# Performance work log

Hardware: AMD Instinct MI355X
Metric: run time of the kernel (lower is better)

The kernel has to match this reference:

```python
import jax, jax.numpy as jnp
import numpy as np

# Mamba2(d_model=256, headdim=32) defaults: d_state=128, d_conv=4, expand=2, ngroups=1, chunk=256
B, CIN, L = 8, 256, 1024
D_MODEL = CIN
D_INNER = 2 * D_MODEL            # expand=2 -> 512
HEADDIM = 32
NHEADS = D_INNER // HEADDIM      # 16
D_STATE = 128
D_CONV = 4
CONV_DIM = D_INNER + 2 * D_STATE             # 768 (ngroups=1)
D_IN_PROJ = 2 * D_INNER + 2 * D_STATE + NHEADS  # 1296
GN_GROUPS = 8
CHUNK = 256
EPS = 1e-5

def setup_inputs():
    key = jax.random.key(0)
    ks = jax.random.split(key, 8)
    x = jax.random.normal(ks[0], (B, CIN, L), jnp.float32)
    W_in = jax.random.normal(ks[1], (D_IN_PROJ, D_MODEL), jnp.float32) * 0.02
    conv_w = jax.random.normal(ks[2], (CONV_DIM, D_CONV), jnp.float32) * 0.2
    conv_b = jax.random.normal(ks[3], (CONV_DIM,), jnp.float32) * 0.02
    dt = jnp.exp(jax.random.uniform(ks[4], (NHEADS,)) * (jnp.log(0.1) - jnp.log(0.001)) + jnp.log(0.001))
    dt_bias = dt + jnp.log(-jnp.expm1(-dt))   # inverse softplus
    A_log = jnp.log(jax.random.uniform(ks[5], (NHEADS,), minval=1.0, maxval=16.0))
    Dp = jnp.ones((NHEADS,), jnp.float32)
    rms_w = jnp.ones((D_INNER,), jnp.float32)
    W_out = jax.random.normal(ks[6], (D_MODEL, D_INNER), jnp.float32) * 0.02
    gn_w = jnp.ones((CIN,), jnp.float32)
    gn_b = jnp.zeros((CIN,), jnp.float32)
    return dict(x=x, W_in=W_in, conv_w=conv_w, conv_b=conv_b, dt_bias=dt_bias,
                A_log=A_log, Dp=Dp, rms_w=rms_w, W_out=W_out, gn_w=gn_w, gn_b=gn_b)

def segsum(a):
    # a: (..., T) -> (..., T, T) with sum_{j<i<=t} a_i on/below diagonal, -inf above
    T = a.shape[-1]
    cs = jnp.cumsum(a, -1)
    d = cs[..., :, None] - cs[..., None, :]
    mask = jnp.tril(jnp.ones((T, T), bool))
    return jnp.where(mask, d, -jnp.inf)

def ssd(X, A, Bm, Cm):
    # X: (b,l,h,p) already dt-scaled; A: (b,l,h) = dt*A_cont; Bm,Cm: (b,l,n) (ngroups=1)
    b, l, h, p = X.shape
    n = Bm.shape[-1]
    c = l // CHUNK
    X = X.reshape(b, c, CHUNK, h, p)
    A = A.reshape(b, c, CHUNK, h).transpose(0, 3, 1, 2)      # (b,h,c,l)
    Bm = Bm.reshape(b, c, CHUNK, n)
    Cm = Cm.reshape(b, c, CHUNK, n)
    A_cs = jnp.cumsum(A, -1)                                  # (b,h,c,l)
    Lmat = jnp.exp(segsum(A))                                 # (b,h,c,l,l)
    Y_diag = jnp.einsum('bcln,bcsn,bhcls,bcshp->bclhp', Cm, Bm, Lmat, X)
    decay_states = jnp.exp(A_cs[..., -1:] - A_cs)             # (b,h,c,l)
    states = jnp.einsum('bcln,bhcl,bclhp->bchpn', Bm, decay_states, X)
    decay_chunk = jnp.exp(segsum(jnp.pad(A_cs[..., -1], ((0, 0), (0, 0), (1, 0)))))  # (b,h,c+1,c+1)
    states = jnp.concatenate([jnp.zeros_like(states[:, :1]), states], axis=1)        # (b,c+1,h,p,n)
    prev = jnp.einsum('bhzc,bchpn->bzhpn', decay_chunk, states)[:, :-1]              # (b,c,h,p,n)
    Y_off = jnp.einsum('bcln,bchpn,bhcl->bclhp', Cm, prev, jnp.exp(A_cs))
    return (Y_diag + Y_off).reshape(b, l, h, p)

def _forward(x, W_in, conv_w, conv_b, dt_bias, A_log, Dp, rms_w, W_out, gn_w, gn_b):
    u = jnp.transpose(x, (0, 2, 1))                           # (B,L,d_model)
    zxbcdt = u @ W_in.T                                       # (B,L,1296)
    z = zxbcdt[..., :D_INNER]
    xBC = zxbcdt[..., D_INNER:D_INNER + CONV_DIM]
    dt = jax.nn.softplus(zxbcdt[..., D_INNER + CONV_DIM:] + dt_bias)  # (B,L,H)
    # causal depthwise conv1d + SiLU
    xpad = jnp.pad(xBC, ((0, 0), (D_CONV - 1, 0), (0, 0)))
    xconv = conv_b + sum(conv_w[:, k] * xpad[:, k:k + L, :] for k in range(D_CONV))
    xconv = jax.nn.silu(xconv)
    xs = xconv[..., :D_INNER].reshape(B, L, NHEADS, HEADDIM)
    Bm = xconv[..., D_INNER:D_INNER + D_STATE]
    Cm = xconv[..., D_INNER + D_STATE:]
    A = -jnp.exp(A_log)                                       # (H,)
    Y = ssd(dt[..., None] * xs, dt * A, Bm, Cm)               # (B,L,H,P)
    Y = Y + xs * Dp[None, None, :, None]
    # gated RMSNorm (norm_before_gate=False): rmsnorm(y * silu(z)) * weight
    y = Y.reshape(B, L, D_INNER) * jax.nn.silu(z)
    y = y * jax.lax.rsqrt(jnp.mean(y * y, -1, keepdims=True) + EPS) * rms_w
    out = jnp.transpose(y @ W_out.T, (0, 2, 1))               # (B,C,L)
    # GroupNorm(8, C) over (channels_per_group, L)
    og = out.reshape(B, GN_GROUPS, CIN // GN_GROUPS, L)
    mu = og.mean((2, 3), keepdims=True)
    var = og.var((2, 3), keepdims=True)
    out = ((og - mu) * jax.lax.rsqrt(var + EPS)).reshape(B, CIN, L)
    out = out * gn_w[None, :, None] + gn_b[None, :, None]
    return out * jnp.tanh(jax.nn.softplus(out))               # Mish

def reference(x, W_in, conv_w, conv_b, dt_bias, A_log, Dp, rms_w, W_out, gn_w, gn_b):
    return _forward(x, W_in, conv_w, conv_b, dt_bias, A_log, Dp, rms_w, W_out, gn_w, gn_b)
```

## Files before the change

### kernel.cpp

```cpp
#include <hip/hip_runtime.h>
#include <hip/hip_bf16.h>
#include <math.h>

#define B_ 8
#define L_ 1024
#define DM 256
#define DI 512
#define HD 32
#define NH 16
#define DS 128
#define CDIM 768
#define NZX 1280
#define CH 256
#define NC 4
#define M_ (B_*L_)
#define EPSV 1e-5f

typedef short bf16x8 __attribute__((ext_vector_type(8)));
typedef float f32x4 __attribute__((ext_vector_type(4)));

#define OFF_ZX   0
#define SZ_ZX    (M_*NZX/2)
#define OFF_XC   (OFF_ZX+SZ_ZX)
#define SZ_XC    (M_*CDIM/2)
#define OFF_DTP  (OFF_XC+SZ_XC)
#define SZ_DTP   (4*M_*NH)
#define OFF_ACS  (OFF_DTP+SZ_DTP)
#define SZ_ACS   (B_*NC*NH*CH)
#define OFF_S0   (OFF_ACS+SZ_ACS)
#define SZ_S0    (B_*NC*CH*CH/2)
#define OFF_ST   (OFF_S0+SZ_S0)
#define SZ_ST    (B_*NC*NH*HD*DS/2)
#define OFF_Y    (OFF_ST+SZ_ST)
#define SZ_Y     (M_*DI/2)
#define OFF_YNB  (OFF_Y+SZ_Y)
#define SZ_YNB   (M_*DI/2)
#define OFF_XBF  (OFF_YNB+SZ_YNB)
#define SZ_XBF   (M_*DM/2)
#define OFF_WBF  (OFF_XBF+SZ_XBF)
#define SZ_WBF   (1296*DM/2)
#define OFF_WOBF (OFF_WBF+SZ_WBF)
#define SZ_WOBF  (DM*DI/2)
#define OFF_GNP  (OFF_WOBF+SZ_WOBF)
#define SZ_GNP   (64*2)
#define OFF_BT   (OFF_GNP+SZ_GNP)
#define SZ_BT    (32*128*256/2)
#define OFF_OUTB (OFF_BT+SZ_BT)
#define SZ_OUTB  (M_*DM/2)

__device__ __forceinline__ ushort f2bf(float v) {
  __hip_bfloat16 h = __float2bfloat16(v);
  return *(ushort*)&h;
}
__device__ __forceinline__ float bf2f(ushort u) {
  return __uint_as_float(((unsigned int)u) << 16);
}
__device__ __forceinline__ float dt_load(const float* __restrict__ dtp, size_t di) {
  float s = dtp[di] + dtp[(size_t)M_*NH + di] + dtp[2*(size_t)M_*NH + di] + dtp[3*(size_t)M_*NH + di];
  return (s > 20.f) ? s : log1pf(expf(s));
}

__device__ __forceinline__ void gload16(const ushort* g, ushort* l) {
  __builtin_amdgcn_global_load_lds(
      (const __attribute__((address_space(1))) unsigned int*)g,
      (__attribute__((address_space(3))) unsigned int*)l,
      16, 0, 0);
}

__global__ __launch_bounds__(256) void k_prep(const float* __restrict__ x,
                                              const float* __restrict__ W_in,
                                              const float* __restrict__ W_out,
                                              const float* __restrict__ dt_bias,
                                              ushort* __restrict__ xbf,
                                              ushort* __restrict__ wbf,
                                              ushort* __restrict__ wobf,
                                              float2* __restrict__ gnp,
                                              float* __restrict__ dtp) {
  __shared__ float Ts[64][65];
  __shared__ float Wd[16][65];
  const int bid = blockIdx.x;
  const int t = threadIdx.x;
  if (bid < 512) {
    const int kt = bid & 3, lt2 = (bid >> 2) & 15, b = bid >> 6;
    const int k0 = kt*64, l0 = lt2*64;
    for (int i = t; i < 1024; i += 256) {
      int kk = i>>4, lw = i&15;
      float4 v = *(const float4*)&x[(size_t)b*DM*L_ + (size_t)(k0+kk)*L_ + l0 + lw*4];
      Ts[kk][lw*4+0] = v.x; Ts[kk][lw*4+1] = v.y;
      Ts[kk][lw*4+2] = v.z; Ts[kk][lw*4+3] = v.w;
    }
    for (int i = t; i < 1024; i += 256) {
      int h = i>>6, kk = i&63;
      Wd[h][kk] = W_in[(size_t)(NZX+h)*DM + k0+kk];
    }
    __syncthreads();
    for (int i = t; i < 512; i += 256) {
      int mm = i>>3, kg = i&7;
      union { ushort u[8]; uint4 q; } pk;
#pragma unroll
      for (int j = 0; j < 8; ++j) pk.u[j] = f2bf(Ts[kg*8+j][mm]);
      *(uint4*)&xbf[(size_t)(b*L_ + l0+mm)*DM + k0 + kg*8] = pk.q;
    }
    const int h = t&15, lg = t>>4;
    const float bias = (kt == 0) ? dt_bias[h] : 0.f;
#pragma unroll
    for (int c = 0; c < 4; ++c) {
      const int ll = lg + c*16;
      float acc = bias;
#pragma unroll 8
      for (int kk = 0; kk < 64; ++kk) acc += Wd[h][kk]*Ts[kk][ll];
      dtp[(size_t)kt*M_*NH + (size_t)(b*L_ + l0+ll)*NH + h] = acc;
    }
  } else if (bid < 512 + 1296) {
    int i = (bid-512)*256 + t;
    if (i < 1296*DM) wbf[i] = f2bf(W_in[i]);
  } else if (bid < 512 + 1296 + 512) {
    int i = (bid-512-1296)*256 + t;
    wobf[i] = f2bf(W_out[i]);
  } else {
    if (t < 64) gnp[t] = make_float2(0.f, 0.f);
  }
}

__global__ __launch_bounds__(256) void k_gemm_in_mfma(const ushort* __restrict__ xbf,
                                                      const ushort* __restrict__ wbf,
                                                      ushort* __restrict__ zxb) {
  __shared__ __attribute__((aligned(16))) ushort As[2][128*32];
  __shared__ __attribute__((aligned(16))) ushort Bs[2][128*32];
  const int tid = threadIdx.x;
  const int n0 = blockIdx.x*128, m0 = blockIdx.y*128;
  const int wave = tid>>6, lane = tid&63;
  const int lr = lane&15, quad = lane>>4;
  const int rA = lane>>2;
  const int cA = (lane&3)*8;
  f32x4 acc[2][8];
#pragma unroll
  for (int mi=0;mi<2;++mi)
#pragma unroll
    for (int ni=0;ni<8;++ni)
#pragma unroll
      for (int r=0;r<4;++r) acc[mi][ni][r] = 0.f;
  auto STAGE = [&](int buf, int k0) {
#pragma unroll
    for (int j = 0; j < 2; ++j) {
      const int ch = 2*wave + j;
      const int row = ch*16 + rA;
      gload16(xbf + (size_t)(m0+row)*DM + k0 + cA, &As[buf][ch*512]);
      gload16(wbf + (size_t)(n0+row)*DM + k0 + cA, &Bs[buf][ch*512]);
    }
  };
  STAGE(0, 0);
#pragma unroll
  for (int i = 0; i < 8; ++i) {
    __syncthreads();
    if (i < 7) STAGE((i+1)&1, (i+1)*32);
    const int cur = i&1;
    bf16x8 af[2], bfr[8];
    af[0] = *(const bf16x8*)&As[cur][(wave*32+lr)*32 + quad*8];
    af[1] = *(const bf16x8*)&As[cur][(wave*32+16+lr)*32 + quad*8];
#pragma unroll
    for (int ni=0;ni<8;++ni) bfr[ni] = *(const bf16x8*)&Bs[cur][(ni*16+lr)*32 + quad*8];
#pragma unroll
    for (int mi=0;mi<2;++mi)
#pragma unroll
      for (int ni=0;ni<8;++ni)
        acc[mi][ni] = __builtin_amdgcn_mfma_f32_16x16x32_bf16(af[mi], bfr[ni], acc[mi][ni], 0, 0, 0);
  }
#pragma unroll
  for (int mi=0;mi<2;++mi) {
    int m = m0 + wave*32 + mi*16 + quad*4;
#pragma unroll
    for (int ni=0;ni<8;++ni) {
      int n = n0 + ni*16 + lr;
#pragma unroll
      for (int r=0;r<4;++r) zxb[(size_t)(m+r)*NZX + n] = f2bf(acc[mi][ni][r]);
    }
  }
}

__global__ __launch_bounds__(256) void k_conv(const ushort* __restrict__ zxb,
                                              const float* __restrict__ cw,
                                              const float* __restrict__ cb,
                                              ushort* __restrict__ xcb,
                                              ushort* __restrict__ btg) {
  const int j = blockIdx.x*256 + threadIdx.x;
  const int m8 = blockIdx.y*8;
  const int l0 = m8 & 1023;
  const int mb = m8 & ~1023;
  const float4 w = *(const float4*)&cw[j*4];
  const float bias = cb[j];
  float v[11];
#pragma unroll
  for (int i = 0; i < 11; ++i) {
    int ll = l0 - 3 + i;
    v[i] = (ll >= 0) ? bf2f(zxb[(size_t)(mb+ll)*NZX + DI + j]) : 0.f;
  }
  union { ushort u[8]; uint4 q; } res;
#pragma unroll
  for (int i = 0; i < 8; ++i) {
    float a = bias + w.x*v[i] + w.y*v[i+1] + w.z*v[i+2] + w.w*v[i+3];
    a = a / (1.f + expf(-a));
    res.u[i] = f2bf(a);
    xcb[(size_t)(mb+l0+i)*CDIM + j] = res.u[i];
  }
  if (j >= DI && j < DI+DS) {
    const int n = j - DI;
    const int bc = (mb >> 10)*NC + (l0 >> 8);
    const int lc = l0 & 255;
    *(uint4*)&btg[((size_t)bc*DS + n)*CH + lc] = res.q;
  }
}

__global__ __launch_bounds__(256) void k_s0st(const ushort* __restrict__ xcb,
                                              const ushort* __restrict__ btg,
                                              const float* __restrict__ dtp,
                                              const float* __restrict__ A_log,
                                              float* __restrict__ acs_g,
                                              ushort* __restrict__ stb,
                                              ushort* __restrict__ S0b) {
  __shared__ float wtot[4];
  __shared__ ushort Xw[32][264];
  const int role = blockIdx.x;
  const int bc = blockIdx.y;
  const int base = bc*CH;
  const int t = threadIdx.x;
  const int wave = t>>6, lane = t&63, lr = lane&15, quad = lane>>4;
  if (role < 10) {
    const int lt = (role>=6) ? 3 : (role>=3) ? 2 : (role>=1) ? 1 : 0;
    const int st = role - lt*(lt+1)/2;
    const int l = lt*64 + wave*16 + lr;
    f32x4 acc[4];
#pragma unroll
    for (int nt = 0; nt < 4; ++nt)
#pragma unroll
      for (int r = 0; r < 4; ++r) acc[nt][r] = 0.f;
#pragma unroll
    for (int ks = 0; ks < 4; ++ks) {
      bf16x8 af = *(const bf16x8*)(xcb + (size_t)(base+l)*CDIM + (DI+DS) + ks*32 + quad*8);
#pragma unroll
      for (int nt = 0; nt < 4; ++nt) {
        bf16x8 bf = *(const bf16x8*)(xcb + (size_t)(base + st*64 + nt*16 + lr)*CDIM + DI + ks*32 + quad*8);
        acc[nt] = __builtin_amdgcn_mfma_f32_16x16x32_bf16(af, bf, acc[nt], 0, 0, 0);
      }
    }
    const bool diag = (lt == st);
#pragma unroll
    for (int nt = 0; nt < 4; ++nt)
#pragma unroll
      for (int r = 0; r < 4; ++r) {
        const int lrow = lt*64 + wave*16 + quad*4 + r;
        const int scol = st*64 + nt*16 + lr;
        ushort v = (!diag || scol <= lrow) ? f2bf(acc[nt][r]) : (ushort)0;
        S0b[((size_t)bc*CH + lrow)*CH + scol] = v;
      }
    return;
  }
  const int h = role - 10;
  float dt_t = dt_load(dtp, (size_t)(base+t)*NH + h);
  float An = -expf(A_log[h]);
  float v = dt_t * An;
#pragma unroll
  for (int off = 1; off < 64; off <<= 1) {
    float u = __shfl_up(v, off);
    if (lane >= off) v += u;
  }
  if (lane == 63) wtot[wave] = v;
  __syncthreads();
  float pre = 0.f, tot = 0.f;
#pragma unroll
  for (int wj = 0; wj < 4; ++wj) {
    float wv = wtot[wj];
    tot += wv;
    if (wj < wave) pre += wv;
  }
  const float a = v + pre;
  const float alast = tot;
  acs_g[((size_t)bc*NH + h)*CH + t] = a;
  float w = expf(alast - a) * dt_t;
  {
    const ushort* xp = xcb + (size_t)(base+t)*CDIM + h*HD;
    ushort tmp[32];
    *(uint4*)&tmp[0]  = *(const uint4*)(xp);
    *(uint4*)&tmp[8]  = *(const uint4*)(xp+8);
    *(uint4*)&tmp[16] = *(const uint4*)(xp+16);
    *(uint4*)&tmp[24] = *(const uint4*)(xp+24);
#pragma unroll
    for (int p = 0; p < 32; ++p) Xw[p][t] = f2bf(bf2f(tmp[p]) * w);
  }
  __syncthreads();
  f32x4 acc2[2][2];
#pragma unroll
  for (int mt=0;mt<2;++mt)
#pragma unroll
    for (int nt=0;nt<2;++nt)
#pragma unroll
      for (int r=0;r<4;++r) acc2[mt][nt][r] = 0.f;
  const ushort* bp = btg + (size_t)bc*DS*CH;
#pragma unroll
  for (int k0 = 0; k0 < CH; k0 += 32) {
    bf16x8 a0 = *(const bf16x8*)&Xw[lr][k0 + quad*8];
    bf16x8 a1 = *(const bf16x8*)&Xw[16+lr][k0 + quad*8];
    bf16x8 b0 = *(const bf16x8*)(bp + (size_t)(wave*32 + lr)*CH + k0 + quad*8);
    bf16x8 b1 = *(const bf16x8*)(bp + (size_t)(wave*32 + 16 + lr)*CH + k0 + quad*8);
    acc2[0][0] = __builtin_amdgcn_mfma_f32_16x16x32_bf16(a0, b0, acc2[0][0], 0,0,0);
    acc2[0][1] = __builtin_amdgcn_mfma_f32_16x16x32_bf16(a0, b1, acc2[0][1], 0,0,0);
    acc2[1][0] = __builtin_amdgcn_mfma_f32_16x16x32_bf16(a1, b0, acc2[1][0], 0,0,0);
    acc2[1][1] = __builtin_amdgcn_mfma_f32_16x16x32_bf16(a1, b1, acc2[1][1], 0,0,0);
  }
  size_t sb = ((size_t)bc*NH + h)*HD*DS;
#pragma unroll
  for (int mt = 0; mt < 2; ++mt)
#pragma unroll
    for (int nt = 0; nt < 2; ++nt)
#pragma unroll
      for (int r = 0; r < 4; ++r)
        stb[sb + (size_t)(mt*16 + quad*4 + r)*DS + wave*32 + nt*16 + lr] = f2bf(acc2[mt][nt][r]);
}

__global__ __launch_bounds__(256) void k_y_mfma(const ushort* __restrict__ xcb,
    const float* __restrict__ dtp, const float* __restrict__ acs_g,
    const ushort* __restrict__ S0b, const ushort* __restrict__ stb,
    const float* __restrict__ Dp, ushort* __restrict__ Yb) {
  __shared__ ushort Xt[32][280];
  __shared__ ushort Xs[32][280];
  __shared__ float acs[CH];
  const int t = threadIdx.x;
  const int bc = blockIdx.x, h = blockIdx.y;
  const int base = bc*CH;
  const int cc = bc & 3, bc4 = bc & ~3;
  acs[t] = acs_g[((size_t)bc*NH + h)*CH + t];
  const float dts_t = dt_load(dtp, (size_t)(base+t)*NH + h);
  ushort tmp[32];
  {
    const ushort* xp = xcb + (size_t)(base+t)*CDIM + h*HD;
    *(uint4*)&tmp[0]  = *(const uint4*)(xp);
    *(uint4*)&tmp[8]  = *(const uint4*)(xp+8);
    *(uint4*)&tmp[16] = *(const uint4*)(xp+16);
    *(uint4*)&tmp[24] = *(const uint4*)(xp+24);
#pragma unroll
    for (int p = 0; p < 32; ++p) Xt[p][t] = tmp[p];
  }
  __syncthreads();
  const float e32 = expf(acs[t & ~31] - acs[t]) * dts_t;
#pragma unroll
  for (int p = 0; p < 32; ++p) Xs[p][t] = f2bf(bf2f(tmp[p]) * e32);
  __syncthreads();
  const int wave = t>>6, lane = t&63, lr = lane&15, quad = lane>>4;
  f32x4 acc[4][2];
#pragma unroll
  for (int mt=0;mt<4;++mt)
#pragma unroll
    for (int nt=0;nt<2;++nt)
#pragma unroll
      for (int r=0;r<4;++r) acc[mt][nt][r] = 0.f;
  if (cc > 0) {
    float fj[3];
    {
      float cum = 0.f;
      for (int j = cc-1; j >= 0; --j) {
        fj[j] = expf(cum);
        cum += acs_g[((size_t)(bc4+j)*NH + h)*CH + (CH-1)];
      }
    }
#pragma unroll
    for (int ks = 0; ks < 4; ++ks) {
      bf16x8 bfr[2];
#pragma unroll
      for (int nt = 0; nt < 2; ++nt) {
        float P[8];
#pragma unroll
        for (int jj = 0; jj < 8; ++jj) P[jj] = 0.f;
        for (int j = 0; j < cc; ++j) {
          bf16x8 sv = *(const bf16x8*)(stb + ((size_t)(bc4+j)*NH + h)*HD*DS
                                       + (size_t)(nt*16+lr)*DS + ks*32 + quad*8);
#pragma unroll
          for (int jj = 0; jj < 8; ++jj) P[jj] += fj[j]*bf2f((ushort)sv[jj]);
        }
        bf16x8 bb;
#pragma unroll
        for (int jj = 0; jj < 8; ++jj) bb[jj] = (short)f2bf(P[jj]);
        bfr[nt] = bb;
      }
#pragma unroll
      for (int mt = 0; mt < 4; ++mt) {
        int l = mt*64 + wave*16 + lr;
        bf16x8 af = *(const bf16x8*)(xcb + (size_t)(base+l)*CDIM + (DI+DS) + ks*32 + quad*8);
        acc[mt][0] = __builtin_amdgcn_mfma_f32_16x16x32_bf16(af, bfr[0], acc[mt][0], 0,0,0);
        acc[mt][1] = __builtin_amdgcn_mfma_f32_16x16x32_bf16(af, bfr[1], acc[mt][1], 0,0,0);
      }
    }
    const float es0 = expf(acs[0]);
#pragma unroll
    for (int mt = 0; mt < 4; ++mt)
#pragma unroll
      for (int nt = 0; nt < 2; ++nt)
#pragma unroll
        for (int r = 0; r < 4; ++r) acc[mt][nt][r] *= es0;
  }
  const int Kw = (12 + wave) >> 1;
  for (int ks = 0; ks <= Kw; ++ks) {
    const int sq = ks*32;
    const bf16x8 xb0 = *(const bf16x8*)&Xs[lr][sq + quad*8];
    const bf16x8 xb1 = *(const bf16x8*)&Xs[16+lr][sq + quad*8];
    const float g = (ks > 0) ? expf(acs[sq] - acs[sq-32]) : 1.f;
#pragma unroll
    for (int mt = 0; mt < 4; ++mt) {
      const int rt = 4*mt + wave;
      if (ks > (rt>>1)) continue;
      if (ks > 0) {
#pragma unroll
        for (int r = 0; r < 4; ++r) { acc[mt][0][r] *= g; acc[mt][1][r] *= g; }
      }
      const int l = mt*64 + wave*16 + lr;
      const bf16x8 sb = *(const bf16x8*)(S0b + ((size_t)bc*CH + l)*CH + sq + quad*8);
      acc[mt][0] = __builtin_amdgcn_mfma_f32_16x16x32_bf16(sb, xb0, acc[mt][0], 0,0,0);
      acc[mt][1] = __builtin_amdgcn_mfma_f32_16x16x32_bf16(sb, xb1, acc[mt][1], 0,0,0);
    }
  }
  const float dph = Dp[h];
#pragma unroll
  for (int mt = 0; mt < 4; ++mt) {
    const int Kmt = (4*mt + wave) >> 1;
    const float aref = acs[32*Kmt];
    const int lb = mt*64 + wave*16 + quad*4;
#pragma unroll
    for (int r = 0; r < 4; ++r) {
      const float e = expf(acs[lb+r] - aref);
#pragma unroll
      for (int nt = 0; nt < 2; ++nt) {
        const int p = nt*16 + lr;
        float xv = bf2f(Xt[p][lb+r]);
        Yb[(size_t)(base+lb+r)*DI + h*HD + p] = f2bf(acc[mt][nt][r]*e + dph*xv);
      }
    }
  }
}

__global__ __launch_bounds__(256) void k_rms(const ushort* __restrict__ zxb,
                                             const ushort* __restrict__ Yb,
                                             const float* __restrict__ rw,
                                             ushort* __restrict__ yn) {
  const int m = blockIdx.x*4 + (threadIdx.x>>6);
  const int lane = threadIdx.x & 63;
  const int c0 = lane*8;
  bf16x8 zv = *(const bf16x8*)(zxb + (size_t)m*NZX + c0);
  bf16x8 yv = *(const bf16x8*)(Yb  + (size_t)m*DI  + c0);
  float y[8];
  float ss = 0.f;
#pragma unroll
  for (int j = 0; j < 8; ++j) {
    float z = bf2f((ushort)zv[j]);
    y[j] = bf2f((ushort)yv[j]) * z / (1.f + expf(-z));
    ss += y[j]*y[j];
  }
#pragma unroll
  for (int off = 1; off < 64; off <<= 1) ss += __shfl_xor(ss, off);
  const float inv = rsqrtf(ss * (1.f/DI) + EPSV);
  float4 w0 = *(const float4*)&rw[c0];
  float4 w1 = *(const float4*)&rw[c0+4];
  const float wv[8] = {w0.x,w0.y,w0.z,w0.w,w1.x,w1.y,w1.z,w1.w};
  union { ushort u[8]; uint4 q; } pk;
#pragma unroll
  for (int j = 0; j < 8; ++j) pk.u[j] = f2bf(y[j] * inv * wv[j]);
  *(uint4*)(yn + (size_t)m*DI + c0) = pk.q;
}

__global__ __launch_bounds__(256) void k_gemm_out_mfma(const ushort* __restrict__ ynbf,
                                                       const ushort* __restrict__ wobf,
                                                       ushort* __restrict__ outb,
                                                       float2* __restrict__ gnp) {
  __shared__ __attribute__((aligned(16))) ushort As[2][64*32];
  __shared__ __attribute__((aligned(16))) ushort Bs[2][128*32];
  __shared__ float red[4][8];
  const int tid = threadIdx.x;
  const int n0 = blockIdx.x*128, m0 = blockIdx.y*64;
  const int wave = tid>>6, lane = tid&63;
  const int lr = lane&15, quad = lane>>4;
  const int rA = lane>>2;
  const int cA = (lane&3)*8;
  f32x4 acc[8];
#pragma unroll
  for (int ni=0;ni<8;++ni)
#pragma unroll
    for (int r=0;r<4;++r) acc[ni][r] = 0.f;
  auto STAGE = [&](int buf, int k0) {
    gload16(ynbf + (size_t)(m0 + wave*16 + rA)*DI + k0 + cA, &As[buf][wave*512]);
#pragma unroll
    for (int j = 0; j < 2; ++j) {
      const int ch = 2*wave + j;
      gload16(wobf + (size_t)(n0 + ch*16 + rA)*DI + k0 + cA, &Bs[buf][ch*512]);
    }
  };
  STAGE(0, 0);
#pragma unroll
  for (int i = 0; i < 16; ++i) {
    __syncthreads();
    if (i < 15) STAGE((i+1)&1, (i+1)*32);
    const int cur = i&1;
    bf16x8 af = *(const bf16x8*)&As[cur][(wave*16+lr)*32 + quad*8];
    bf16x8 bfr[8];
#pragma unroll
    for (int ni=0;ni<8;++ni) bfr[ni] = *(const bf16x8*)&Bs[cur][(ni*16+lr)*32 + quad*8];
#pragma unroll
    for (int ni=0;ni<8;++ni)
      acc[ni] = __builtin_amdgcn_mfma_f32_16x16x32_bf16(af, bfr[ni], acc[ni], 0, 0, 0);
  }
  const int b = m0 >> 10, l0 = m0 & 1023;
  float sg[4] = {0.f,0.f,0.f,0.f}, sq2[4] = {0.f,0.f,0.f,0.f};
#pragma unroll
  for (int ni=0;ni<8;++ni) {
    int n = n0 + ni*16 + lr;
    union { ushort u[4]; uint2 q; } pk;
#pragma unroll
    for (int r=0;r<4;++r) pk.u[r] = f2bf(acc[ni][r]);
    *(uint2*)&outb[(size_t)b*DM*L_ + (size_t)n*L_ + l0 + wave*16 + quad*4] = pk.q;
    float ps = acc[ni][0]+acc[ni][1]+acc[ni][2]+acc[ni][3];
    float pq = acc[ni][0]*acc[ni][0]+acc[ni][1]*acc[ni][1]
             + acc[ni][2]*acc[ni][2]+acc[ni][3]*acc[ni][3];
    sg[ni>>1] += ps; sq2[ni>>1] += pq;
  }
#pragma unroll
  for (int g = 0; g < 4; ++g)
#pragma unroll
    for (int off = 32; off > 0; off >>= 1) {
      sg[g]  += __shfl_down(sg[g],  off);
      sq2[g] += __shfl_down(sq2[g], off);
    }
  if (lane == 0) {
#pragma unroll
    for (int g = 0; g < 4; ++g) { red[wave][g] = sg[g]; red[wave][4+g] = sq2[g]; }
  }
  __syncthreads();
  if (tid == 0) {
    int g0 = b*8 + (n0>>5);
#pragma unroll
    for (int g = 0; g < 4; ++g) {
      float S = red[0][g]+red[1][g]+red[2][g]+red[3][g];
      float Q = red[0][4+g]+red[1][4+g]+red[2][4+g]+red[3][4+g];
      atomicAdd(&gnp[g0+g].x, S);
      atomicAdd(&gnp[g0+g].y, Q);
    }
  }
}

__global__ __launch_bounds__(256) void k_gn_apply(const float2* __restrict__ gnp,
                                                  const float* __restrict__ gw,
                                                  const float* __restrict__ gb,
                                                  const ushort* __restrict__ ob,
                                                  float* __restrict__ o) {
  const int ch = blockIdx.x & 255, b = blockIdx.x >> 8;
  const int t = threadIdx.x;
  float2 p = gnp[b*8 + (ch>>5)];
  const float mean = p.x * (1.f/(32.f*L_));
  const float var  = p.y * (1.f/(32.f*L_)) - mean*mean;
  const float inv  = rsqrtf(var + EPSV);
  const float w = gw[ch], bb = gb[ch];
  size_t base = (size_t)blockIdx.x * L_;
  ushort4 v = *(const ushort4*)&ob[base + t*4];
  float r[4] = {bf2f(v.x), bf2f(v.y), bf2f(v.z), bf2f(v.w)};
#pragma unroll
  for (int j = 0; j < 4; ++j) {
    float u = (r[j] - mean) * inv * w + bb;
    float m;
    if (u > 15.f) m = u;
    else {
      float e = expf(u);
      float a = 1.f + e;
      float a2 = a*a;
      m = u * (a2 - 1.f) / (a2 + 1.f);
    }
    r[j] = m;
  }
  *(float4*)&o[base + t*4] = make_float4(r[0], r[1], r[2], r[3]);
}

extern "C" void kernel_launch(void* const* d_in, const int* in_sizes, int n_in,
                              void* d_out, int out_size, void* d_ws, size_t ws_size,
                              hipStream_t stream) {
  const float* x       = (const float*)d_in[0];
  const float* W_in    = (const float*)d_in[1];
  const float* conv_w  = (const float*)d_in[2];
  const float* conv_b  = (const float*)d_in[3];
  const float* dt_bias = (const float*)d_in[4];
  const float* A_log   = (const float*)d_in[5];
  const float* Dp      = (const float*)d_in[6];
  const float* rms_w   = (const float*)d_in[7];
  const float* W_out   = (const float*)d_in[8];
  const float* gn_w    = (const float*)d_in[9];
  const float* gn_b    = (const float*)d_in[10];
  float* out = (float*)d_out;
  float* ws  = (float*)d_ws;

  ushort* zxb   = (ushort*)(ws + OFF_ZX);
  ushort* xcb   = (ushort*)(ws + OFF_XC);
  float*  dtp   = ws + OFF_DTP;
  float*  acs   = ws + OFF_ACS;
  ushort* S0b   = (ushort*)(ws + OFF_S0);
  ushort* stb   = (ushort*)(ws + OFF_ST);
  ushort* Ybb   = (ushort*)(ws + OFF_Y);
  ushort* ynbf  = (ushort*)(ws + OFF_YNB);
  ushort* xbf   = (ushort*)(ws + OFF_XBF);
  ushort* wbf   = (ushort*)(ws + OFF_WBF);
  ushort* wobf  = (ushort*)(ws + OFF_WOBF);
  float2* gnp   = (float2*)(ws + OFF_GNP);
  ushort* btg   = (ushort*)(ws + OFF_BT);
  ushort* outb  = (ushort*)(ws + OFF_OUTB);

  k_prep         <<<dim3(512+1296+512+1), 256, 0, stream>>>(x, W_in, W_out, dt_bias,
                                                            xbf, wbf, wobf, gnp, dtp);
  k_gemm_in_mfma <<<dim3(NZX/128, M_/128), 256, 0, stream>>>(xbf, wbf, zxb);
  k_conv         <<<dim3(3, M_/8), 256, 0, stream>>>(zxb, conv_w, conv_b, xcb, btg);
  k_s0st         <<<dim3(26, B_*NC), 256, 0, stream>>>(xcb, btg, dtp, A_log, acs, stb, S0b);
  k_y_mfma       <<<dim3(B_*NC, NH), 256, 0, stream>>>(xcb, dtp, acs, S0b, stb, Dp, Ybb);
  k_rms          <<<dim3(M_/4), 256, 0, stream>>>(zxb, Ybb, rms_w, ynbf);
  k_gemm_out_mfma<<<dim3(DM/128, M_/64), 256, 0, stream>>>(ynbf, wobf, outb, gnp);
  k_gn_apply     <<<dim3(B_*DM), 256, 0, stream>>>(gnp, gn_w, gn_b, outb, out);
}
```

Baseline: 176.0 us.

## Fuse gated RMSNorm into output GEMM and transpose-store via shared memory

```diff
diff --git a/kernel.cpp b/kernel.cpp
--- a/kernel.cpp
+++ b/kernel.cpp
@@ -325,7 +325,7 @@
   __shared__ ushort Xs[32][280];
   __shared__ float acs[CH];
   const int t = threadIdx.x;
-  const int bc = blockIdx.x, h = blockIdx.y;
+  const int h = blockIdx.x, bc = blockIdx.y;
   const int base = bc*CH;
   const int cc = bc & 3, bc4 = bc & ~3;
   acs[t] = acs_g[((size_t)bc*NH + h)*CH + t];
@@ -436,91 +436,90 @@
   }
 }
 
-__global__ __launch_bounds__(256) void k_rms(const ushort* __restrict__ zxb,
-                                             const ushort* __restrict__ Yb,
-                                             const float* __restrict__ rw,
-                                             ushort* __restrict__ yn) {
-  const int m = blockIdx.x*4 + (threadIdx.x>>6);
-  const int lane = threadIdx.x & 63;
-  const int c0 = lane*8;
-  bf16x8 zv = *(const bf16x8*)(zxb + (size_t)m*NZX + c0);
-  bf16x8 yv = *(const bf16x8*)(Yb  + (size_t)m*DI  + c0);
-  float y[8];
-  float ss = 0.f;
-#pragma unroll
-  for (int j = 0; j < 8; ++j) {
-    float z = bf2f((ushort)zv[j]);
-    y[j] = bf2f((ushort)yv[j]) * z / (1.f + expf(-z));
-    ss += y[j]*y[j];
-  }
-#pragma unroll
-  for (int off = 1; off < 64; off <<= 1) ss += __shfl_xor(ss, off);
-  const float inv = rsqrtf(ss * (1.f/DI) + EPSV);
-  float4 w0 = *(const float4*)&rw[c0];
-  float4 w1 = *(const float4*)&rw[c0+4];
-  const float wv[8] = {w0.x,w0.y,w0.z,w0.w,w1.x,w1.y,w1.z,w1.w};
-  union { ushort u[8]; uint4 q; } pk;
-#pragma unroll
-  for (int j = 0; j < 8; ++j) pk.u[j] = f2bf(y[j] * inv * wv[j]);
-  *(uint4*)(yn + (size_t)m*DI + c0) = pk.q;
-}
-
-__global__ __launch_bounds__(256) void k_gemm_out_mfma(const ushort* __restrict__ ynbf,
-                                                       const ushort* __restrict__ wobf,
-                                                       ushort* __restrict__ outb,
-                                                       float2* __restrict__ gnp) {
-  __shared__ __attribute__((aligned(16))) ushort As[2][64*32];
+__global__ __launch_bounds__(256) void k_out_fused(const ushort* __restrict__ zxb,
+                                                   const ushort* __restrict__ Yb,
+                                                   const float* __restrict__ rw,
+                                                   const ushort* __restrict__ wobf,
+                                                   ushort* __restrict__ outb,
+                                                   float2* __restrict__ gnp) {
+  __shared__ __attribute__((aligned(16))) ushort As[32*512];
   __shared__ __attribute__((aligned(16))) ushort Bs[2][128*32];
-  __shared__ float red[4][8];
+  __shared__ __attribute__((aligned(16))) ushort Tr[128*40];
   const int tid = threadIdx.x;
-  const int n0 = blockIdx.x*128, m0 = blockIdx.y*64;
   const int wave = tid>>6, lane = tid&63;
   const int lr = lane&15, quad = lane>>4;
-  const int rA = lane>>2;
-  const int cA = (lane&3)*8;
-  f32x4 acc[8];
-#pragma unroll
-  for (int ni=0;ni<8;++ni)
-#pragma unroll
-    for (int r=0;r<4;++r) acc[ni][r] = 0.f;
+  const int n0 = blockIdx.x*128, m0 = blockIdx.y*32;
+  const int rB = lane>>2, cB = (lane&3)*8;
   auto STAGE = [&](int buf, int k0) {
-    gload16(ynbf + (size_t)(m0 + wave*16 + rA)*DI + k0 + cA, &As[buf][wave*512]);
 #pragma unroll
     for (int j = 0; j < 2; ++j) {
       const int ch = 2*wave + j;
-      gload16(wobf + (size_t)(n0 + ch*16 + rA)*DI + k0 + cA, &Bs[buf][ch*512]);
+      gload16(wobf + (size_t)(n0 + ch*16 + rB)*DI + k0 + cB, &Bs[buf][ch*512]);
     }
   };
   STAGE(0, 0);
+  {
+    const int c0 = lane*8;
+    float4 w0 = *(const float4*)&rw[c0];
+    float4 w1 = *(const float4*)&rw[c0+4];
+    const float wv[8] = {w0.x,w0.y,w0.z,w0.w,w1.x,w1.y,w1.z,w1.w};
+    for (int i = 0; i < 8; ++i) {
+      const int R = wave*8 + i;
+      const int m = m0 + R;
+      bf16x8 zv = *(const bf16x8*)(zxb + (size_t)m*NZX + c0);
+      bf16x8 yv = *(const bf16x8*)(Yb  + (size_t)m*DI  + c0);
+      float y[8]; float ss = 0.f;
+#pragma unroll
+      for (int j = 0; j < 8; ++j) {
+        float z = bf2f((ushort)zv[j]);
+        y[j] = bf2f((ushort)yv[j]) * z / (1.f + expf(-z));
+        ss += y[j]*y[j];
+      }
+#pragma unroll
+      for (int off = 1; off < 64; off <<= 1) ss += __shfl_xor(ss, off);
+      const float inv = rsqrtf(ss * (1.f/DI) + EPSV);
+      union { ushort u[8]; uint4 q; } pk;
+#pragma unroll
+      for (int j = 0; j < 8; ++j) pk.u[j] = f2bf(y[j] * inv * wv[j]);
+      *(uint4*)&As[R*512 + (c0 ^ ((R&7)<<3))] = pk.q;
+    }
+  }
+  f32x4 acc[4];
+#pragma unroll
+  for (int ni=0;ni<4;++ni)
+#pragma unroll
+    for (int r=0;r<4;++r) acc[ni][r] = 0.f;
+  const int mf = wave>>1, nf = wave&1;
+  const int RA = mf*16 + lr;
 #pragma unroll
   for (int i = 0; i < 16; ++i) {
     __syncthreads();
     if (i < 15) STAGE((i+1)&1, (i+1)*32);
     const int cur = i&1;
-    bf16x8 af = *(const bf16x8*)&As[cur][(wave*16+lr)*32 + quad*8];
-    bf16x8 bfr[8];
-#pragma unroll
-    for (int ni=0;ni<8;++ni) bfr[ni] = *(const bf16x8*)&Bs[cur][(ni*16+lr)*32 + quad*8];
-#pragma unroll
-    for (int ni=0;ni<8;++ni)
+    bf16x8 af = *(const bf16x8*)&As[RA*512 + ((i*32 + quad*8) ^ ((RA&7)<<3))];
+    bf16x8 bfr[4];
+#pragma unroll
+    for (int ni=0;ni<4;++ni)
+      bfr[ni] = *(const bf16x8*)&Bs[cur][(nf*64 + ni*16 + lr)*32 + quad*8];
+#pragma unroll
+    for (int ni=0;ni<4;++ni)
       acc[ni] = __builtin_amdgcn_mfma_f32_16x16x32_bf16(af, bfr[ni], acc[ni], 0, 0, 0);
   }
   const int b = m0 >> 10, l0 = m0 & 1023;
-  float sg[4] = {0.f,0.f,0.f,0.f}, sq2[4] = {0.f,0.f,0.f,0.f};
-#pragma unroll
-  for (int ni=0;ni<8;++ni) {
-    int n = n0 + ni*16 + lr;
-    union { ushort u[4]; uint2 q; } pk;
-#pragma unroll
-    for (int r=0;r<4;++r) pk.u[r] = f2bf(acc[ni][r]);
-    *(uint2*)&outb[(size_t)b*DM*L_ + (size_t)n*L_ + l0 + wave*16 + quad*4] = pk.q;
-    float ps = acc[ni][0]+acc[ni][1]+acc[ni][2]+acc[ni][3];
-    float pq = acc[ni][0]*acc[ni][0]+acc[ni][1]*acc[ni][1]
-             + acc[ni][2]*acc[ni][2]+acc[ni][3]*acc[ni][3];
-    sg[ni>>1] += ps; sq2[ni>>1] += pq;
-  }
-#pragma unroll
-  for (int g = 0; g < 4; ++g)
+  float sg[2] = {0.f,0.f}, sq2[2] = {0.f,0.f};
+#pragma unroll
+  for (int ni=0;ni<4;++ni) {
+    const int n = nf*64 + ni*16 + lr;
+#pragma unroll
+    for (int r=0;r<4;++r) {
+      const float v = acc[ni][r];
+      Tr[n*40 + mf*16 + quad*4 + r] = f2bf(v);
+      sg[ni>>1]  += v;
+      sq2[ni>>1] += v*v;
+    }
+  }
+#pragma unroll
+  for (int g = 0; g < 2; ++g)
 #pragma unroll
     for (int off = 32; off > 0; off >>= 1) {
       sg[g]  += __shfl_down(sg[g],  off);
@@ -528,18 +527,18 @@
     }
   if (lane == 0) {
 #pragma unroll
-    for (int g = 0; g < 4; ++g) { red[wave][g] = sg[g]; red[wave][4+g] = sq2[g]; }
+    for (int g = 0; g < 2; ++g) {
+      const int gi = b*8 + (n0>>5) + nf*2 + g;
+      atomicAdd(&gnp[gi].x, sg[g]);
+      atomicAdd(&gnp[gi].y, sq2[g]);
+    }
   }
   __syncthreads();
-  if (tid == 0) {
-    int g0 = b*8 + (n0>>5);
-#pragma unroll
-    for (int g = 0; g < 4; ++g) {
-      float S = red[0][g]+red[1][g]+red[2][g]+red[3][g];
-      float Q = red[0][4+g]+red[1][4+g]+red[2][4+g]+red[3][4+g];
-      atomicAdd(&gnp[g0+g].x, S);
-      atomicAdd(&gnp[g0+g].y, Q);
-    }
+#pragma unroll
+  for (int it = 0; it < 2; ++it) {
+    const int w = it*256 + tid;
+    const int n = w >> 2, mo = (w&3)*8;
+    *(uint4*)&outb[(size_t)b*DM*L_ + (size_t)(n0+n)*L_ + l0 + mo] = *(const uint4*)&Tr[n*40 + mo];
   }
 }
 
@@ -598,7 +597,6 @@
   ushort* S0b   = (ushort*)(ws + OFF_S0);
   ushort* stb   = (ushort*)(ws + OFF_ST);
   ushort* Ybb   = (ushort*)(ws + OFF_Y);
-  ushort* ynbf  = (ushort*)(ws + OFF_YNB);
   ushort* xbf   = (ushort*)(ws + OFF_XBF);
   ushort* wbf   = (ushort*)(ws + OFF_WBF);
   ushort* wobf  = (ushort*)(ws + OFF_WOBF);
@@ -611,8 +609,7 @@
   k_gemm_in_mfma <<<dim3(NZX/128, M_/128), 256, 0, stream>>>(xbf, wbf, zxb);
   k_conv         <<<dim3(3, M_/8), 256, 0, stream>>>(zxb, conv_w, conv_b, xcb, btg);
   k_s0st         <<<dim3(26, B_*NC), 256, 0, stream>>>(xcb, btg, dtp, A_log, acs, stb, S0b);
-  k_y_mfma       <<<dim3(B_*NC, NH), 256, 0, stream>>>(xcb, dtp, acs, S0b, stb, Dp, Ybb);
-  k_rms          <<<dim3(M_/4), 256, 0, stream>>>(zxb, Ybb, rms_w, ynbf);
-  k_gemm_out_mfma<<<dim3(DM/128, M_/64), 256, 0, stream>>>(ynbf, wobf, outb, gnp);
+  k_y_mfma       <<<dim3(NH, B_*NC), 256, 0, stream>>>(xcb, dtp, acs, S0b, stb, Dp, Ybb);
+  k_out_fused    <<<dim3(DM/128, M_/32), 256, 0, stream>>>(zxb, Ybb, rms_w, wobf, outb, gnp);
   k_gn_apply     <<<dim3(B_*DM), 256, 0, stream>>>(gnp, gn_w, gn_b, outb, out);
 }
```

Measured after the change: 204.5 us. 16.2% more time.

## Retile output GEMM to 64x64 blocks with 2x2 wave layout and swizzled LDS

Applied to the files above, without the earlier changes.

```diff
diff --git a/kernel.cpp b/kernel.cpp
--- a/kernel.cpp
+++ b/kernel.cpp
@@ -469,77 +469,82 @@
                                                        const ushort* __restrict__ wobf,
                                                        ushort* __restrict__ outb,
                                                        float2* __restrict__ gnp) {
-  __shared__ __attribute__((aligned(16))) ushort As[2][64*32];
-  __shared__ __attribute__((aligned(16))) ushort Bs[2][128*32];
-  __shared__ float red[4][8];
+  __shared__ __attribute__((aligned(16))) ushort As[2][64*64];
+  __shared__ __attribute__((aligned(16))) ushort Bs[2][64*64];
   const int tid = threadIdx.x;
-  const int n0 = blockIdx.x*128, m0 = blockIdx.y*64;
+  const int n0 = blockIdx.x*64, m0 = blockIdx.y*64;
   const int wave = tid>>6, lane = tid&63;
   const int lr = lane&15, quad = lane>>4;
-  const int rA = lane>>2;
-  const int cA = (lane&3)*8;
-  f32x4 acc[8];
-#pragma unroll
-  for (int ni=0;ni<8;++ni)
-#pragma unroll
-    for (int r=0;r<4;++r) acc[ni][r] = 0.f;
+  const int rA = lane>>3;
+  const int cA = ((lane&7) ^ rA)*8;
+  f32x4 acc[2][2];
+#pragma unroll
+  for (int mi=0;mi<2;++mi)
+#pragma unroll
+    for (int ni=0;ni<2;++ni)
+#pragma unroll
+      for (int r=0;r<4;++r) acc[mi][ni][r] = 0.f;
   auto STAGE = [&](int buf, int k0) {
-    gload16(ynbf + (size_t)(m0 + wave*16 + rA)*DI + k0 + cA, &As[buf][wave*512]);
 #pragma unroll
     for (int j = 0; j < 2; ++j) {
       const int ch = 2*wave + j;
-      gload16(wobf + (size_t)(n0 + ch*16 + rA)*DI + k0 + cA, &Bs[buf][ch*512]);
+      const int row = ch*8 + rA;
+      gload16(ynbf + (size_t)(m0+row)*DI + k0 + cA, &As[buf][ch*512]);
+      gload16(wobf + (size_t)(n0+row)*DI + k0 + cA, &Bs[buf][ch*512]);
     }
   };
   STAGE(0, 0);
-#pragma unroll
-  for (int i = 0; i < 16; ++i) {
+  const int mw = wave>>1, nw = wave&1;
+#pragma unroll
+  for (int i = 0; i < 8; ++i) {
     __syncthreads();
-    if (i < 15) STAGE((i+1)&1, (i+1)*32);
+    if (i < 7) STAGE((i+1)&1, (i+1)*64);
     const int cur = i&1;
-    bf16x8 af = *(const bf16x8*)&As[cur][(wave*16+lr)*32 + quad*8];
-    bf16x8 bfr[8];
-#pragma unroll
-    for (int ni=0;ni<8;++ni) bfr[ni] = *(const bf16x8*)&Bs[cur][(ni*16+lr)*32 + quad*8];
-#pragma unroll
-    for (int ni=0;ni<8;++ni)
-      acc[ni] = __builtin_amdgcn_mfma_f32_16x16x32_bf16(af, bfr[ni], acc[ni], 0, 0, 0);
+#pragma unroll
+    for (int ks = 0; ks < 2; ++ks) {
+      bf16x8 af[2], bfr[2];
+#pragma unroll
+      for (int mi = 0; mi < 2; ++mi) {
+        const int R = mw*32 + mi*16 + lr;
+        af[mi] = *(const bf16x8*)&As[cur][R*64 + (((ks*4+quad) ^ (R&7))*8)];
+      }
+#pragma unroll
+      for (int ni = 0; ni < 2; ++ni) {
+        const int R = nw*32 + ni*16 + lr;
+        bfr[ni] = *(const bf16x8*)&Bs[cur][R*64 + (((ks*4+quad) ^ (R&7))*8)];
+      }
+#pragma unroll
+      for (int mi=0;mi<2;++mi)
+#pragma unroll
+        for (int ni=0;ni<2;++ni)
+          acc[mi][ni] = __builtin_amdgcn_mfma_f32_16x16x32_bf16(af[mi], bfr[ni], acc[mi][ni], 0, 0, 0);
+    }
   }
   const int b = m0 >> 10, l0 = m0 & 1023;
-  float sg[4] = {0.f,0.f,0.f,0.f}, sq2[4] = {0.f,0.f,0.f,0.f};
-#pragma unroll
-  for (int ni=0;ni<8;++ni) {
-    int n = n0 + ni*16 + lr;
-    union { ushort u[4]; uint2 q; } pk;
-#pragma unroll
-    for (int r=0;r<4;++r) pk.u[r] = f2bf(acc[ni][r]);
-    *(uint2*)&outb[(size_t)b*DM*L_ + (size_t)n*L_ + l0 + wave*16 + quad*4] = pk.q;
-    float ps = acc[ni][0]+acc[ni][1]+acc[ni][2]+acc[ni][3];
-    float pq = acc[ni][0]*acc[ni][0]+acc[ni][1]*acc[ni][1]
-             + acc[ni][2]*acc[ni][2]+acc[ni][3]*acc[ni][3];
-    sg[ni>>1] += ps; sq2[ni>>1] += pq;
-  }
-#pragma unroll
-  for (int g = 0; g < 4; ++g)
-#pragma unroll
-    for (int off = 32; off > 0; off >>= 1) {
-      sg[g]  += __shfl_down(sg[g],  off);
-      sq2[g] += __shfl_down(sq2[g], off);
-    }
+  float sg = 0.f, sq2 = 0.f;
+#pragma unroll
+  for (int mi=0;mi<2;++mi)
+#pragma unroll
+    for (int ni=0;ni<2;++ni) {
+      const int n = n0 + nw*32 + ni*16 + lr;
+      union { ushort u[4]; uint2 q; } pk;
+#pragma unroll
+      for (int r=0;r<4;++r) {
+        const float v = acc[mi][ni][r];
+        pk.u[r] = f2bf(v);
+        sg += v; sq2 += v*v;
+      }
+      *(uint2*)&outb[(size_t)b*DM*L_ + (size_t)n*L_ + l0 + mw*32 + mi*16 + quad*4] = pk.q;
+    }
+#pragma unroll
+  for (int off = 32; off > 0; off >>= 1) {
+    sg  += __shfl_down(sg,  off);
+    sq2 += __shfl_down(sq2, off);
+  }
   if (lane == 0) {
-#pragma unroll
-    for (int g = 0; g < 4; ++g) { red[wave][g] = sg[g]; red[wave][4+g] = sq2[g]; }
-  }
-  __syncthreads();
-  if (tid == 0) {
-    int g0 = b*8 + (n0>>5);
-#pragma unroll
-    for (int g = 0; g < 4; ++g) {
-      float S = red[0][g]+red[1][g]+red[2][g]+red[3][g];
-      float Q = red[0][4+g]+red[1][4+g]+red[2][4+g]+red[3][4+g];
-      atomicAdd(&gnp[g0+g].x, S);
-      atomicAdd(&gnp[g0+g].y, Q);
-    }
+    const int gi = b*8 + (n0>>5) + nw;
+    atomicAdd(&gnp[gi].x, sg);
+    atomicAdd(&gnp[gi].y, sq2);
   }
 }
 
@@ -613,6 +618,6 @@
   k_s0st         <<<dim3(26, B_*NC), 256, 0, stream>>>(xcb, btg, dtp, A_log, acs, stb, S0b);
   k_y_mfma       <<<dim3(B_*NC, NH), 256, 0, stream>>>(xcb, dtp, acs, S0b, stb, Dp, Ybb);
   k_rms          <<<dim3(M_/4), 256, 0, stream>>>(zxb, Ybb, rms_w, ynbf);
-  k_gemm_out_mfma<<<dim3(DM/128, M_/64), 256, 0, stream>>>(ynbf, wobf, outb, gnp);
+  k_gemm_out_mfma<<<dim3(DM/64, M_/64), 256, 0, stream>>>(ynbf, wobf, outb, gnp);
   k_gn_apply     <<<dim3(B_*DM), 256, 0, stream>>>(gnp, gn_w, gn_b, outb, out);
 }
```

Result: no change. 179.4 us (+1.9%).

## Split Y kernel row tiles across two blocks with balanced triangle pairing; vectorize weight casts

Applied to the files above, without the earlier changes.

```diff
diff --git a/kernel.cpp b/kernel.cpp
--- a/kernel.cpp
+++ b/kernel.cpp
@@ -111,12 +111,22 @@
       for (int kk = 0; kk < 64; ++kk) acc += Wd[h][kk]*Ts[kk][ll];
       dtp[(size_t)kt*M_*NH + (size_t)(b*L_ + l0+ll)*NH + h] = acc;
     }
-  } else if (bid < 512 + 1296) {
-    int i = (bid-512)*256 + t;
-    if (i < 1296*DM) wbf[i] = f2bf(W_in[i]);
-  } else if (bid < 512 + 1296 + 512) {
-    int i = (bid-512-1296)*256 + t;
-    wobf[i] = f2bf(W_out[i]);
+  } else if (bid < 512 + 162) {
+    const int i = ((bid-512)*256 + t)*8;
+    float4 a = *(const float4*)&W_in[i];
+    float4 b = *(const float4*)&W_in[i+4];
+    union { ushort u[8]; uint4 q; } pk;
+    pk.u[0]=f2bf(a.x); pk.u[1]=f2bf(a.y); pk.u[2]=f2bf(a.z); pk.u[3]=f2bf(a.w);
+    pk.u[4]=f2bf(b.x); pk.u[5]=f2bf(b.y); pk.u[6]=f2bf(b.z); pk.u[7]=f2bf(b.w);
+    *(uint4*)&wbf[i] = pk.q;
+  } else if (bid < 512 + 162 + 64) {
+    const int i = ((bid-512-162)*256 + t)*8;
+    float4 a = *(const float4*)&W_out[i];
+    float4 b = *(const float4*)&W_out[i+4];
+    union { ushort u[8]; uint4 q; } pk;
+    pk.u[0]=f2bf(a.x); pk.u[1]=f2bf(a.y); pk.u[2]=f2bf(a.z); pk.u[3]=f2bf(a.w);
+    pk.u[4]=f2bf(b.x); pk.u[5]=f2bf(b.y); pk.u[6]=f2bf(b.z); pk.u[7]=f2bf(b.w);
+    *(uint4*)&wobf[i] = pk.q;
   } else {
     if (t < 64) gnp[t] = make_float2(0.f, 0.f);
   }
@@ -325,7 +335,7 @@
   __shared__ ushort Xs[32][280];
   __shared__ float acs[CH];
   const int t = threadIdx.x;
-  const int bc = blockIdx.x, h = blockIdx.y;
+  const int bc = blockIdx.x, h = blockIdx.y, hf = blockIdx.z;
   const int base = bc*CH;
   const int cc = bc & 3, bc4 = bc & ~3;
   acs[t] = acs_g[((size_t)bc*NH + h)*CH + t];
@@ -346,13 +356,16 @@
   for (int p = 0; p < 32; ++p) Xs[p][t] = f2bf(bf2f(tmp[p]) * e32);
   __syncthreads();
   const int wave = t>>6, lane = t&63, lr = lane&15, quad = lane>>4;
-  f32x4 acc[4][2];
-#pragma unroll
-  for (int mt=0;mt<4;++mt)
+  const int t0 = hf*4 + wave, t1 = 15 - t0;
+  const int K0 = t0>>1, K1 = t1>>1;
+  const int l0r = t0*16 + lr, l1r = t1*16 + lr;
+  f32x4 acc[2][2];
+#pragma unroll
+  for (int ti=0;ti<2;++ti)
 #pragma unroll
     for (int nt=0;nt<2;++nt)
 #pragma unroll
-      for (int r=0;r<4;++r) acc[mt][nt][r] = 0.f;
+      for (int r=0;r<4;++r) acc[ti][nt][r] = 0.f;
   if (cc > 0) {
     float fj[3];
     {
@@ -381,48 +394,50 @@
         for (int jj = 0; jj < 8; ++jj) bb[jj] = (short)f2bf(P[jj]);
         bfr[nt] = bb;
       }
-#pragma unroll
-      for (int mt = 0; mt < 4; ++mt) {
-        int l = mt*64 + wave*16 + lr;
-        bf16x8 af = *(const bf16x8*)(xcb + (size_t)(base+l)*CDIM + (DI+DS) + ks*32 + quad*8);
-        acc[mt][0] = __builtin_amdgcn_mfma_f32_16x16x32_bf16(af, bfr[0], acc[mt][0], 0,0,0);
-        acc[mt][1] = __builtin_amdgcn_mfma_f32_16x16x32_bf16(af, bfr[1], acc[mt][1], 0,0,0);
-      }
+      bf16x8 af0 = *(const bf16x8*)(xcb + (size_t)(base+l0r)*CDIM + (DI+DS) + ks*32 + quad*8);
+      bf16x8 af1 = *(const bf16x8*)(xcb + (size_t)(base+l1r)*CDIM + (DI+DS) + ks*32 + quad*8);
+      acc[0][0] = __builtin_amdgcn_mfma_f32_16x16x32_bf16(af0, bfr[0], acc[0][0], 0,0,0);
+      acc[0][1] = __builtin_amdgcn_mfma_f32_16x16x32_bf16(af0, bfr[1], acc[0][1], 0,0,0);
+      acc[1][0] = __builtin_amdgcn_mfma_f32_16x16x32_bf16(af1, bfr[0], acc[1][0], 0,0,0);
+      acc[1][1] = __builtin_amdgcn_mfma_f32_16x16x32_bf16(af1, bfr[1], acc[1][1], 0,0,0);
     }
     const float es0 = expf(acs[0]);
 #pragma unroll
-    for (int mt = 0; mt < 4; ++mt)
+    for (int ti = 0; ti < 2; ++ti)
 #pragma unroll
       for (int nt = 0; nt < 2; ++nt)
 #pragma unroll
-        for (int r = 0; r < 4; ++r) acc[mt][nt][r] *= es0;
-  }
-  const int Kw = (12 + wave) >> 1;
-  for (int ks = 0; ks <= Kw; ++ks) {
+        for (int r = 0; r < 4; ++r) acc[ti][nt][r] *= es0;
+  }
+  for (int ks = 0; ks <= K1; ++ks) {
     const int sq = ks*32;
     const bf16x8 xb0 = *(const bf16x8*)&Xs[lr][sq + quad*8];
     const bf16x8 xb1 = *(const bf16x8*)&Xs[16+lr][sq + quad*8];
     const float g = (ks > 0) ? expf(acs[sq] - acs[sq-32]) : 1.f;
-#pragma unroll
-    for (int mt = 0; mt < 4; ++mt) {
-      const int rt = 4*mt + wave;
-      if (ks > (rt>>1)) continue;
+    if (ks <= K0) {
       if (ks > 0) {
 #pragma unroll
-        for (int r = 0; r < 4; ++r) { acc[mt][0][r] *= g; acc[mt][1][r] *= g; }
+        for (int r = 0; r < 4; ++r) { acc[0][0][r] *= g; acc[0][1][r] *= g; }
       }
-      const int l = mt*64 + wave*16 + lr;
-      const bf16x8 sb = *(const bf16x8*)(S0b + ((size_t)bc*CH + l)*CH + sq + quad*8);
-      acc[mt][0] = __builtin_amdgcn_mfma_f32_16x16x32_bf16(sb, xb0, acc[mt][0], 0,0,0);
-      acc[mt][1] = __builtin_amdgcn_mfma_f32_16x16x32_bf16(sb, xb1, acc[mt][1], 0,0,0);
-    }
+      const bf16x8 sb = *(const bf16x8*)(S0b + ((size_t)bc*CH + l0r)*CH + sq + quad*8);
+      acc[0][0] = __builtin_amdgcn_mfma_f32_16x16x32_bf16(sb, xb0, acc[0][0], 0,0,0);
+      acc[0][1] = __builtin_amdgcn_mfma_f32_16x16x32_bf16(sb, xb1, acc[0][1], 0,0,0);
+    }
+    if (ks > 0) {
+#pragma unroll
+      for (int r = 0; r < 4; ++r) { acc[1][0][r] *= g; acc[1][1][r] *= g; }
+    }
+    const bf16x8 sb1 = *(const bf16x8*)(S0b + ((size_t)bc*CH + l1r)*CH + sq + quad*8);
+    acc[1][0] = __builtin_amdgcn_mfma_f32_16x16x32_bf16(sb1, xb0, acc[1][0], 0,0,0);
+    acc[1][1] = __builtin_amdgcn_mfma_f32_16x16x32_bf16(sb1, xb1, acc[1][1], 0,0,0);
   }
   const float dph = Dp[h];
 #pragma unroll
-  for (int mt = 0; mt < 4; ++mt) {
-    const int Kmt = (4*mt + wave) >> 1;
-    const float aref = acs[32*Kmt];
-    const int lb = mt*64 + wave*16 + quad*4;
+  for (int ti = 0; ti < 2; ++ti) {
+    const int tt = ti ? t1 : t0;
+    const int Kt = tt>>1;
+    const float aref = acs[32*Kt];
+    const int lb = tt*16 + quad*4;
 #pragma unroll
     for (int r = 0; r < 4; ++r) {
       const float e = expf(acs[lb+r] - aref);
@@ -430,7 +445,7 @@
       for (int nt = 0; nt < 2; ++nt) {
         const int p = nt*16 + lr;
         float xv = bf2f(Xt[p][lb+r]);
-        Yb[(size_t)(base+lb+r)*DI + h*HD + p] = f2bf(acc[mt][nt][r]*e + dph*xv);
+        Yb[(size_t)(base+lb+r)*DI + h*HD + p] = f2bf(acc[ti][nt][r]*e + dph*xv);
       }
     }
   }
@@ -606,12 +621,12 @@
   ushort* btg   = (ushort*)(ws + OFF_BT);
   ushort* outb  = (ushort*)(ws + OFF_OUTB);
 
-  k_prep         <<<dim3(512+1296+512+1), 256, 0, stream>>>(x, W_in, W_out, dt_bias,
-                                                            xbf, wbf, wobf, gnp, dtp);
+  k_prep         <<<dim3(512+162+64+1), 256, 0, stream>>>(x, W_in, W_out, dt_bias,
+                                                          xbf, wbf, wobf, gnp, dtp);
   k_gemm_in_mfma <<<dim3(NZX/128, M_/128), 256, 0, stream>>>(xbf, wbf, zxb);
   k_conv         <<<dim3(3, M_/8), 256, 0, stream>>>(zxb, conv_w, conv_b, xcb, btg);
   k_s0st         <<<dim3(26, B_*NC), 256, 0, stream>>>(xcb, btg, dtp, A_log, acs, stb, S0b);
-  k_y_mfma       <<<dim3(B_*NC, NH), 256, 0, stream>>>(xcb, dtp, acs, S0b, stb, Dp, Ybb);
+  k_y_mfma       <<<dim3(B_*NC, NH, 2), 256, 0, stream>>>(xcb, dtp, acs, S0b, stb, Dp, Ybb);
   k_rms          <<<dim3(M_/4), 256, 0, stream>>>(zxb, Ybb, rms_w, ynbf);
   k_gemm_out_mfma<<<dim3(DM/128, M_/64), 256, 0, stream>>>(ynbf, wobf, outb, gnp);
   k_gn_apply     <<<dim3(B_*DM), 256, 0, stream>>>(gnp, gn_w, gn_b, outb, out);
```

Result: slower. 179.7 us (+2.1%).
